# Kernel optimization log

Measured on AMD Instinct MI355X. Metric: run time of the kernel, lower is better.

## Reference

```python
import jax, jax.numpy as jnp
import numpy as np
from jax import lax

D_MODEL = 64      # feature_dim
D_STATE = 16      # state_dim
D_CONV = 4        # conv_dim
EXPAND = 2
D_INNER = EXPAND * D_MODEL          # 128
DT_RANK = (D_MODEL + 15) // 16      # ceil(d_model/16) = 4, mamba default
IN_DIM = 64
LN_EPS = 1e-3                        # keras LayerNormalization default epsilon


def setup_inputs() -> dict:
    key = jax.random.key(0)
    ks = jax.random.split(key, 12)
    B, L = 16, 8192
    s = 0.02
    x = jax.random.normal(ks[0], (B, L, IN_DIM), jnp.float32)
    W_in = jax.random.normal(ks[1], (IN_DIM, D_MODEL), jnp.float32) * s
    b_in = jnp.zeros((D_MODEL,), jnp.float32)
    in_proj_w = jax.random.normal(ks[2], (D_MODEL, 2 * D_INNER), jnp.float32) * s
    conv_w = jax.random.normal(ks[3], (D_INNER, D_CONV), jnp.float32) * 0.1
    conv_b = jnp.zeros((D_INNER,), jnp.float32)
    x_proj_w = jax.random.normal(ks[4], (D_INNER, DT_RANK + 2 * D_STATE), jnp.float32) * s
    dt_proj_w = jax.random.normal(ks[5], (DT_RANK, D_INNER), jnp.float32) * (DT_RANK ** -0.5)
    # dt bias init so softplus(dt) lands roughly in [dt_min, dt_max]
    dt = jnp.exp(jax.random.uniform(ks[6], (D_INNER,)) * (np.log(0.1) - np.log(0.001)) + np.log(0.001))
    dt_proj_b = dt + jnp.log(-jnp.expm1(-dt))  # inverse softplus
    A_log = jnp.log(jnp.broadcast_to(jnp.arange(1, D_STATE + 1, dtype=jnp.float32), (D_INNER, D_STATE)))
    D_skip = jnp.ones((D_INNER,), jnp.float32)
    out_proj_w = jax.random.normal(ks[7], (D_INNER, D_MODEL), jnp.float32) * s
    ln_gamma = jnp.ones((D_MODEL,), jnp.float32)
    ln_beta = jnp.zeros((D_MODEL,), jnp.float32)
    return {"x": x, "W_in": W_in, "b_in": b_in, "in_proj_w": in_proj_w,
            "conv_w": conv_w, "conv_b": conv_b, "x_proj_w": x_proj_w,
            "dt_proj_w": dt_proj_w, "dt_proj_b": dt_proj_b, "A_log": A_log,
            "D_skip": D_skip, "out_proj_w": out_proj_w,
            "ln_gamma": ln_gamma, "ln_beta": ln_beta}


def reference(x, W_in, b_in, in_proj_w, conv_w, conv_b, x_proj_w,
              dt_proj_w, dt_proj_b, A_log, D_skip, out_proj_w, ln_gamma, ln_beta):
    B, L, _ = x.shape
    # Conv1D kernel_size=1 input projection
    xin = x @ W_in + b_in                          # [B,L,D_MODEL]
    # --- Mamba ---
    xz = xin @ in_proj_w                           # [B,L,2*D_INNER]
    xc, z = xz[..., :D_INNER], xz[..., D_INNER:]
    # causal depthwise conv (groups=d_inner, padding=d_conv-1, crop to L)
    xp = jnp.pad(xc, ((0, 0), (D_CONV - 1, 0), (0, 0)))
    xconv = conv_b
    for k in range(D_CONV):
        xconv = xconv + xp[:, k:k + L, :] * conv_w[:, k]
    u = jax.nn.silu(xconv)                         # [B,L,D_INNER]
    dbc = u @ x_proj_w                             # [B,L,DT_RANK+2*D_STATE]
    dt = jax.nn.softplus(dbc[..., :DT_RANK] @ dt_proj_w + dt_proj_b)   # [B,L,D_INNER]
    Bm = dbc[..., DT_RANK:DT_RANK + D_STATE]       # [B,L,D_STATE]
    Cm = dbc[..., DT_RANK + D_STATE:]              # [B,L,D_STATE]
    A = -jnp.exp(A_log)                            # [D_INNER,D_STATE]

    def step(h, xs):
        dt_t, b_t, c_t, u_t = xs                   # [B,Di],[B,Ds],[B,Ds],[B,Di]
        dA = jnp.exp(dt_t[:, :, None] * A)         # [B,Di,Ds]
        h = dA * h + (dt_t * u_t)[:, :, None] * b_t[:, None, :]
        y = jnp.einsum('bds,bs->bd', h, c_t)
        return h, y

    xs = (jnp.swapaxes(dt, 0, 1), jnp.swapaxes(Bm, 0, 1),
          jnp.swapaxes(Cm, 0, 1), jnp.swapaxes(u, 0, 1))
    h0 = jnp.zeros((B, D_INNER, D_STATE), x.dtype)
    _, ys = lax.scan(step, h0, xs)                 # ys: [L,B,D_INNER]
    y = jnp.swapaxes(ys, 0, 1) + u * D_skip
    y = y * jax.nn.silu(z)
    h_out = y @ out_proj_w                         # [B,L,D_MODEL]
    # residual + LayerNorm
    res = h_out + xin
    mu = jnp.mean(res, axis=-1, keepdims=True)
    var = jnp.mean(jnp.square(res - mu), axis=-1, keepdims=True)
    return ln_gamma * (res - mu) * lax.rsqrt(var + LN_EPS) + ln_beta
```

## Files before the change

kernel.cpp:

```cpp
#include <hip/hip_runtime.h>
#include <hip/hip_bf16.h>

#define B_SZ   16
#define L_SZ   8192
#define DM     64
#define DI     128
#define NCH    128
#define CLEN   64
#define CH     64
#define RT     80
#define PA     72
#define PU     136
#define PC     132
#define LN_EPS 1e-3f

typedef float  f4 __attribute__((ext_vector_type(4)));
typedef short  s8 __attribute__((ext_vector_type(8)));
typedef unsigned short u16;
typedef unsigned int   u32;
#define MFMA16 __builtin_amdgcn_mfma_f32_16x16x32_bf16

__device__ __forceinline__ u16 f2bfu(float f) {
    u32 u = __float_as_uint(f);
    return (u16)((u + 0x7FFFu + ((u >> 16) & 1u)) >> 16);
}
__device__ __forceinline__ u32 pk2bf(float a, float b) {
    return (u32)f2bfu(a) | ((u32)f2bfu(b) << 16);
}
__device__ __forceinline__ float bflo(u32 u) { return __uint_as_float(u << 16); }
__device__ __forceinline__ float bfhi(u32 u) { return __uint_as_float(u & 0xFFFF0000u); }
__device__ __forceinline__ float bfu2f(u16 h) { return __uint_as_float((u32)h << 16); }
__device__ __forceinline__ float fsig(float v) {
    return __builtin_amdgcn_rcpf(1.f + __expf(-v));
}
__device__ __forceinline__ float fsp(float v) {
    return fmaxf(v, 0.f) + __logf(1.f + __expf(-fabsf(v)));
}

__global__ __launch_bounds__(256) void k_prep(
    const float* __restrict__ W_in, const float* __restrict__ in_proj,
    const float* __restrict__ x_proj, const float* __restrict__ Wout,
    u16* __restrict__ Wf1, u16* __restrict__ Wf2,
    u16* __restrict__ Wf3, u16* __restrict__ Wf4)
{
    const int tid = threadIdx.x;
    for (int g = tid; g < 512; g += 256) {
        int lane = g & 63, ks = (g >> 6) & 1, nt = g >> 7;
        int n = nt * 16 + (lane & 15), kb = ks * 32 + (lane >> 4) * 8;
        for (int j = 0; j < 8; j++) Wf1[g * 8 + j] = f2bfu(W_in[(kb + j) * 64 + n]);
    }
    for (int g = tid; g < 2048; g += 256) {
        int lane = g & 63, ks = (g >> 6) & 1, nt = g >> 7;
        int n = nt * 16 + (lane & 15), kb = ks * 32 + (lane >> 4) * 8;
        for (int j = 0; j < 8; j++) Wf2[g * 8 + j] = f2bfu(in_proj[(kb + j) * 256 + n]);
    }
    for (int g = tid; g < 768; g += 256) {
        int lane = g & 63, ks = (g >> 6) & 3, nt = g >> 8;
        int n = nt * 16 + (lane & 15), kb = ks * 32 + (lane >> 4) * 8;
        for (int j = 0; j < 8; j++)
            Wf3[g * 8 + j] = f2bfu(n < 36 ? x_proj[(kb + j) * 36 + n] : 0.f);
    }
    for (int g = tid; g < 1024; g += 256) {
        int lane = g & 63, ks = (g >> 6) & 3, nt = g >> 8;
        int n = nt * 16 + (lane & 15), kb = ks * 32 + (lane >> 4) * 8;
        for (int j = 0; j < 8; j++) Wf4[g * 8 + j] = f2bfu(Wout[(kb + j) * 64 + n]);
    }
}

__global__ __launch_bounds__(256) void k_frontend(
    const float* __restrict__ x, const float* __restrict__ b_in,
    const float* __restrict__ conv_w, const float* __restrict__ conv_b,
    const u16* __restrict__ Wf1, const u16* __restrict__ Wf2, const u16* __restrict__ Wf3,
    float* __restrict__ xin_g, u16* __restrict__ u_g, float* __restrict__ dtr_g,
    float* __restrict__ B_g, float* __restrict__ C_g, u16* __restrict__ sz_g)
{
    __shared__ __align__(16) char sm[41088];
    u16*   smA   = (u16*)sm;
    u16*   smB   = (u16*)(sm + 11520);
    u16*   smU   = (u16*)sm;
    float* smDtr = (float*)(sm + 17408);
    u16*   smC   = (u16*)(sm + 23040);

    const int tid = threadIdx.x;
    const int w = tid >> 6, lane = tid & 63;
    const int n16 = lane & 15, quad = lane >> 4;
    const int b = blockIdx.y, c0 = blockIdx.x * CH;
    const long long tokbase = (long long)b * L_SZ + c0;

    for (int idx = tid; idx < RT * 16; idx += 256) {
        int r = idx >> 4, c4 = idx & 15;
        int l = c0 - 3 + r;
        float4 v = make_float4(0.f, 0.f, 0.f, 0.f);
        if (r < 67 && l >= 0)
            v = *(const float4*)(x + ((long long)b * L_SZ + l) * 64 + c4 * 4);
        *(uint2*)((char*)smA + r * 144 + c4 * 8) = make_uint2(pk2bf(v.x, v.y), pk2bf(v.z, v.w));
    }
    __syncthreads();

    {
        s8 b0 = *(const s8*)(Wf1 + ((w * 2 + 0) * 64 + lane) * 8);
        s8 b1 = *(const s8*)(Wf1 + ((w * 2 + 1) * 64 + lane) * 8);
        float bias = b_in[w * 16 + n16];
        for (int m = 0; m < 5; m++) {
            int ar = m * 16 + n16;
            s8 a0 = *(const s8*)(smA + ar * PA + quad * 8);
            s8 a1 = *(const s8*)(smA + ar * PA + 32 + quad * 8);
            f4 acc = {0.f, 0.f, 0.f, 0.f};
            acc = MFMA16(a0, b0, acc, 0, 0, 0);
            acc = MFMA16(a1, b1, acc, 0, 0, 0);
#pragma unroll
            for (int reg = 0; reg < 4; reg++) {
                int rr = m * 16 + quad * 4 + reg;
                float v = acc[reg] + bias;
                smB[rr * PA + w * 16 + n16] = f2bfu(v);
                if (rr >= 3 && rr < 67)
                    xin_g[(tokbase + rr - 3) * 64 + w * 16 + n16] = v;
            }
        }
    }
    __syncthreads();

    {
        s8 bf[4][2];
#pragma unroll
        for (int i = 0; i < 4; i++)
#pragma unroll
            for (int ks = 0; ks < 2; ks++)
                bf[i][ks] = *(const s8*)(Wf2 + (((w * 4 + i) * 2 + ks) * 64 + lane) * 8);
        for (int m = 0; m < 5; m++) {
            int ar = m * 16 + n16;
            s8 a0 = *(const s8*)(smB + ar * PA + quad * 8);
            s8 a1 = *(const s8*)(smB + ar * PA + 32 + quad * 8);
#pragma unroll
            for (int i = 0; i < 4; i++) {
                f4 acc = {0.f, 0.f, 0.f, 0.f};
                acc = MFMA16(a0, bf[i][0], acc, 0, 0, 0);
                acc = MFMA16(a1, bf[i][1], acc, 0, 0, 0);
                int cg = (w * 4 + i) * 16 + n16;
#pragma unroll
                for (int reg = 0; reg < 4; reg++) {
                    int rr = m * 16 + quad * 4 + reg;
                    float v = acc[reg];
                    if (cg < 128) {
                        if (rr < 67) {
                            int l = c0 - 3 + rr;
                            smC[rr * PC + cg] = f2bfu(l >= 0 ? v : 0.f);
                        }
                    } else if (rr >= 3 && rr < 67) {
                        sz_g[(tokbase + rr - 3) * 128 + (cg - 128)] = f2bfu(v * fsig(v));
                    }
                }
            }
        }
    }
    __syncthreads();

    {
        const int d2 = lane * 2, ctb = w * 16;
        float4 cw0 = ((const float4*)conv_w)[d2];
        float4 cw1 = ((const float4*)conv_w)[d2 + 1];
        float cb0 = conv_b[d2], cb1 = conv_b[d2 + 1];
        u32 r0 = *(const u32*)((char*)smC + (ctb + 0) * 264 + lane * 4);
        u32 r1 = *(const u32*)((char*)smC + (ctb + 1) * 264 + lane * 4);
        u32 r2 = *(const u32*)((char*)smC + (ctb + 2) * 264 + lane * 4);
#pragma unroll 4
        for (int j = 0; j < 16; j++) {
            int ct = ctb + j;
            u32 r3 = *(const u32*)((char*)smC + (ct + 3) * 264 + lane * 4);
            float v0 = cb0 + bflo(r0) * cw0.x + bflo(r1) * cw0.y + bflo(r2) * cw0.z + bflo(r3) * cw0.w;
            float v1 = cb1 + bfhi(r0) * cw1.x + bfhi(r1) * cw1.y + bfhi(r2) * cw1.z + bfhi(r3) * cw1.w;
            u32 pk = pk2bf(v0 * fsig(v0), v1 * fsig(v1));
            *(u32*)(u_g + (tokbase + ct) * 128 + d2) = pk;
            *(u32*)(smU + ct * PU + d2) = pk;
            r0 = r1; r1 = r2; r2 = r3;
        }
    }
    __syncthreads();

    {
        s8 bf3[3][4];
#pragma unroll
        for (int nt = 0; nt < 3; nt++)
#pragma unroll
            for (int ks = 0; ks < 4; ks++)
                bf3[nt][ks] = *(const s8*)(Wf3 + ((nt * 4 + ks) * 64 + lane) * 8);
        f4 acc[3] = {{0.f,0.f,0.f,0.f},{0.f,0.f,0.f,0.f},{0.f,0.f,0.f,0.f}};
        int ar = w * 16 + n16;
#pragma unroll
        for (int ks = 0; ks < 4; ks++) {
            s8 a = *(const s8*)(smU + ar * PU + ks * 32 + quad * 8);
#pragma unroll
            for (int nt = 0; nt < 3; nt++) acc[nt] = MFMA16(a, bf3[nt][ks], acc[nt], 0, 0, 0);
        }
#pragma unroll
        for (int nt = 0; nt < 3; nt++) {
            int c = nt * 16 + n16;
#pragma unroll
            for (int reg = 0; reg < 4; reg++) {
                int rr = w * 16 + quad * 4 + reg;
                float v = acc[nt][reg];
                long long t = tokbase + rr;
                if (c < 4)       smDtr[rr * 4 + c] = v;
                else if (c < 20) B_g[t * 16 + (c - 4)] = v;
                else if (c < 36) C_g[t * 16 + (c - 20)] = v;
            }
        }
    }
    __syncthreads();

    if (tid < 64)
        *(float4*)(dtr_g + (tokbase + tid) * 4) = *(const float4*)(smDtr + tid * 4);
}

__global__ __launch_bounds__(128) void k_scan1(
    const float* __restrict__ dtr_g, const u16* __restrict__ u_g,
    const float* __restrict__ B_g, const float* __restrict__ A_log,
    const float* __restrict__ dt_w, const float* __restrict__ dt_b,
    float* __restrict__ hl_ws, float* __restrict__ sdt_ws)
{
    __shared__ __align__(16) float smQ[CLEN * 4];
    __shared__ __align__(16) float smBs[CLEN * 16];

    const int d = threadIdx.x, c = blockIdx.x, b = blockIdx.y;
    const long long tok0 = (long long)b * L_SZ + (long long)c * CLEN;

    {
        const float4* srcB = (const float4*)(B_g + tok0 * 16);
        float4* dstB = (float4*)smBs;
        dstB[d] = srcB[d];
        dstB[d + 128] = srcB[d + 128];
        if (d < 64) ((float4*)smQ)[d] = ((const float4*)(dtr_g + tok0 * 4))[d];
    }
    __syncthreads();

    const float w0 = dt_w[d], w1 = dt_w[128 + d], w2 = dt_w[256 + d], w3 = dt_w[384 + d];
    const float bdt = dt_b[d];

    float A[16];
#pragma unroll
    for (int s = 0; s < 16; s++) A[s] = -__expf(A_log[d * 16 + s]);
    const float A0 = A[0];
    bool chain = true;
#pragma unroll
    for (int s = 1; s < 16; s++)
        chain = chain && (fabsf(A[s] - (float)(s + 1) * A0) <= 1e-4f * fabsf(A[s]));

    float h[16];
#pragma unroll
    for (int s = 0; s < 16; s++) h[s] = 0.f;
    float sdt = 0.f;

    if (chain) {
        for (int i = 0; i < CLEN; i++) {
            float4 q = *(const float4*)(smQ + i * 4);
            float dtv = fsp(bdt + q.x * w0 + q.y * w1 + q.z * w2 + q.w * w3);
            float uv  = bfu2f(u_g[(tok0 + i) * 128 + d]);
            float4 b0 = *(const float4*)(smBs + i * 16);
            float4 b1 = *(const float4*)(smBs + i * 16 + 4);
            float4 b2 = *(const float4*)(smBs + i * 16 + 8);
            float4 b3 = *(const float4*)(smBs + i * 16 + 12);
            float Bv[16] = { b0.x, b0.y, b0.z, b0.w, b1.x, b1.y, b1.z, b1.w,
                             b2.x, b2.y, b2.z, b2.w, b3.x, b3.y, b3.z, b3.w };
            float du = dtv * uv;  sdt += dtv;
            float p = __expf(dtv * A0), dA = p;
            h[0] = dA * h[0] + du * Bv[0];
#pragma unroll
            for (int s = 1; s < 16; s++) { dA *= p; h[s] = dA * h[s] + du * Bv[s]; }
        }
    } else {
        for (int i = 0; i < CLEN; i++) {
            float4 q = *(const float4*)(smQ + i * 4);
            float dtv = fsp(bdt + q.x * w0 + q.y * w1 + q.z * w2 + q.w * w3);
            float uv  = bfu2f(u_g[(tok0 + i) * 128 + d]);
            float4 b0 = *(const float4*)(smBs + i * 16);
            float4 b1 = *(const float4*)(smBs + i * 16 + 4);
            float4 b2 = *(const float4*)(smBs + i * 16 + 8);
            float4 b3 = *(const float4*)(smBs + i * 16 + 12);
            float Bv[16] = { b0.x, b0.y, b0.z, b0.w, b1.x, b1.y, b1.z, b1.w,
                             b2.x, b2.y, b2.z, b2.w, b3.x, b3.y, b3.z, b3.w };
            float du = dtv * uv;  sdt += dtv;
#pragma unroll
            for (int s = 0; s < 16; s++) h[s] = __expf(dtv * A[s]) * h[s] + du * Bv[s];
        }
    }

    float4* hp4 = (float4*)(hl_ws + (((long long)b * NCH + c) * 128 + d) * 16);
    hp4[0] = make_float4(h[0], h[1], h[2], h[3]);
    hp4[1] = make_float4(h[4], h[5], h[6], h[7]);
    hp4[2] = make_float4(h[8], h[9], h[10], h[11]);
    hp4[3] = make_float4(h[12], h[13], h[14], h[15]);
    sdt_ws[((long long)b * NCH + c) * 128 + d] = sdt;
}

__global__ __launch_bounds__(256) void k_combine(
    const float* __restrict__ A_log, const float* __restrict__ hl_ws,
    const float* __restrict__ sdt_ws, float* __restrict__ hin_ws)
{
    const int tid = threadIdx.x, lane = tid & 63;
    const int seg = tid & 3;
    const int sIdx = blockIdx.x * 64 + (tid >> 2);
    const int b = sIdx >> 11, rem = sIdx & 2047, d = rem >> 4;
    const float A = -__expf(A_log[rem]);
    const int cBeg = seg * 32;
    const long long hlBase  = ((long long)b * NCH) * 2048 + rem;
    const long long sdtBase = ((long long)b * NCH) * 128 + d;

    float hloc = 0.f, ssum = 0.f;
#pragma unroll 4
    for (int c = cBeg; c < cBeg + 32; c++) {
        float sd = sdt_ws[sdtBase + (long long)c * 128];
        ssum += sd;
        hloc = __expf(A * sd) * hloc + hl_ws[hlBase + (long long)c * 2048];
    }

    float H = 0.f;
    const int gbase = lane & ~3;
#pragma unroll
    for (int k = 0; k < 3; k++) {
        float hs = __shfl(hloc, gbase + k, 64);
        float ss = __shfl(ssum, gbase + k, 64);
        if (k < seg) H = hs + H * __expf(A * ss);
    }

    float h = H;
#pragma unroll 4
    for (int c = cBeg; c < cBeg + 32; c++) {
        hin_ws[hlBase + (long long)c * 2048] = h;
        float sd = sdt_ws[sdtBase + (long long)c * 128];
        h = __expf(A * sd) * h + hl_ws[hlBase + (long long)c * 2048];
    }
}

__global__ __launch_bounds__(128) void k_scan3(
    const float* __restrict__ dtr_g, const u16* __restrict__ u_g,
    const float* __restrict__ B_g, const float* __restrict__ C_g,
    const u16* __restrict__ sz_g, const float* __restrict__ A_log,
    const float* __restrict__ dt_w, const float* __restrict__ dt_b,
    const float* __restrict__ D_skip, const float* __restrict__ hin_ws,
    u16* __restrict__ y_g)
{
    __shared__ __align__(16) float smQ[CLEN * 4];
    __shared__ __align__(16) float smBs[CLEN * 16];
    __shared__ __align__(16) float smCs[CLEN * 16];

    const int d = threadIdx.x, c = blockIdx.x, b = blockIdx.y;
    const long long tok0 = (long long)b * L_SZ + (long long)c * CLEN;

    {
        const float4* srcB = (const float4*)(B_g + tok0 * 16);
        const float4* srcC = (const float4*)(C_g + tok0 * 16);
        ((float4*)smBs)[d] = srcB[d];
        ((float4*)smBs)[d + 128] = srcB[d + 128];
        ((float4*)smCs)[d] = srcC[d];
        ((float4*)smCs)[d + 128] = srcC[d + 128];
        if (d < 64) ((float4*)smQ)[d] = ((const float4*)(dtr_g + tok0 * 4))[d];
    }
    __syncthreads();

    const float w0 = dt_w[d], w1 = dt_w[128 + d], w2 = dt_w[256 + d], w3 = dt_w[384 + d];
    const float bdt = dt_b[d];

    float A[16];
#pragma unroll
    for (int s = 0; s < 16; s++) A[s] = -__expf(A_log[d * 16 + s]);
    const float A0 = A[0];
    bool chain = true;
#pragma unroll
    for (int s = 1; s < 16; s++)
        chain = chain && (fabsf(A[s] - (float)(s + 1) * A0) <= 1e-4f * fabsf(A[s]));

    float h[16];
    {
        const float4* hp = (const float4*)(hin_ws + (((long long)b * NCH + c) * 128 + d) * 16);
        float4 h0 = hp[0], h1 = hp[1], h2 = hp[2], h3 = hp[3];
        h[0]=h0.x; h[1]=h0.y; h[2]=h0.z; h[3]=h0.w;
        h[4]=h1.x; h[5]=h1.y; h[6]=h1.z; h[7]=h1.w;
        h[8]=h2.x; h[9]=h2.y; h[10]=h2.z; h[11]=h2.w;
        h[12]=h3.x; h[13]=h3.y; h[14]=h3.z; h[15]=h3.w;
    }
    const float Dv = D_skip[d];

    if (chain) {
        for (int i = 0; i < CLEN; i++) {
            float4 q = *(const float4*)(smQ + i * 4);
            float dtv = fsp(bdt + q.x * w0 + q.y * w1 + q.z * w2 + q.w * w3);
            float uv  = bfu2f(u_g[(tok0 + i) * 128 + d]);
            float4 b0 = *(const float4*)(smBs + i * 16);
            float4 b1 = *(const float4*)(smBs + i * 16 + 4);
            float4 b2 = *(const float4*)(smBs + i * 16 + 8);
            float4 b3 = *(const float4*)(smBs + i * 16 + 12);
            float Bv[16] = { b0.x, b0.y, b0.z, b0.w, b1.x, b1.y, b1.z, b1.w,
                             b2.x, b2.y, b2.z, b2.w, b3.x, b3.y, b3.z, b3.w };
            float4 c0v = *(const float4*)(smCs + i * 16);
            float4 c1v = *(const float4*)(smCs + i * 16 + 4);
            float4 c2v = *(const float4*)(smCs + i * 16 + 8);
            float4 c3v = *(const float4*)(smCs + i * 16 + 12);
            float Cv[16] = { c0v.x, c0v.y, c0v.z, c0v.w, c1v.x, c1v.y, c1v.z, c1v.w,
                             c2v.x, c2v.y, c2v.z, c2v.w, c3v.x, c3v.y, c3v.z, c3v.w };
            float du = dtv * uv;
            float p = __expf(dtv * A0), dA = p;
            h[0] = dA * h[0] + du * Bv[0];
            float ysum = h[0] * Cv[0];
#pragma unroll
            for (int s = 1; s < 16; s++) {
                dA *= p;
                h[s] = dA * h[s] + du * Bv[s];
                ysum += h[s] * Cv[s];
            }
            float szv = bfu2f(sz_g[(tok0 + i) * 128 + d]);
            y_g[(tok0 + i) * 128 + d] = f2bfu((ysum + uv * Dv) * szv);
        }
    } else {
        for (int i = 0; i < CLEN; i++) {
            float4 q = *(const float4*)(smQ + i * 4);
            float dtv = fsp(bdt + q.x * w0 + q.y * w1 + q.z * w2 + q.w * w3);
            float uv  = bfu2f(u_g[(tok0 + i) * 128 + d]);
            float4 b0 = *(const float4*)(smBs + i * 16);
            float4 b1 = *(const float4*)(smBs + i * 16 + 4);
            float4 b2 = *(const float4*)(smBs + i * 16 + 8);
            float4 b3 = *(const float4*)(smBs + i * 16 + 12);
            float Bv[16] = { b0.x, b0.y, b0.z, b0.w, b1.x, b1.y, b1.z, b1.w,
                             b2.x, b2.y, b2.z, b2.w, b3.x, b3.y, b3.z, b3.w };
            float4 c0v = *(const float4*)(smCs + i * 16);
            float4 c1v = *(const float4*)(smCs + i * 16 + 4);
            float4 c2v = *(const float4*)(smCs + i * 16 + 8);
            float4 c3v = *(const float4*)(smCs + i * 16 + 12);
            float Cv[16] = { c0v.x, c0v.y, c0v.z, c0v.w, c1v.x, c1v.y, c1v.z, c1v.w,
                             c2v.x, c2v.y, c2v.z, c2v.w, c3v.x, c3v.y, c3v.z, c3v.w };
            float du = dtv * uv;
            float ysum = 0.f;
#pragma unroll
            for (int s = 0; s < 16; s++) {
                h[s] = __expf(dtv * A[s]) * h[s] + du * Bv[s];
                ysum += h[s] * Cv[s];
            }
            float szv = bfu2f(sz_g[(tok0 + i) * 128 + d]);
            y_g[(tok0 + i) * 128 + d] = f2bfu((ysum + uv * Dv) * szv);
        }
    }
}

__global__ __launch_bounds__(256) void k_epilogue(
    const u16* __restrict__ y_g, const float* __restrict__ xin_g,
    const u16* __restrict__ Wf4, const float* __restrict__ gamma,
    const float* __restrict__ beta, float* __restrict__ out)
{
    __shared__ __align__(16) char sm[34048];
    u16*   yA  = (u16*)sm;
    float* smR = (float*)(sm + 17408);

    const int tid = threadIdx.x;
    const int w = tid >> 6, lane = tid & 63;
    const int n16 = lane & 15, quad = lane >> 4;
    const long long t0 = (long long)blockIdx.x * 64;

    for (int idx = tid; idx < 64 * 64; idx += 256) {
        int r = idx >> 6, cp = idx & 63;
        u32 v = ((const u32*)y_g)[(t0 + r) * 64 + cp];
        *(u32*)((char*)yA + r * 272 + cp * 4) = v;
    }
    __syncthreads();

    {
        s8 bf[4];
#pragma unroll
        for (int ks = 0; ks < 4; ks++)
            bf[ks] = *(const s8*)(Wf4 + ((w * 4 + ks) * 64 + lane) * 8);
#pragma unroll
        for (int m = 0; m < 4; m++) {
            int ar = m * 16 + n16;
            f4 acc = {0.f, 0.f, 0.f, 0.f};
#pragma unroll
            for (int ks = 0; ks < 4; ks++) {
                s8 a = *(const s8*)(yA + ar * PU + ks * 32 + quad * 8);
                acc = MFMA16(a, bf[ks], acc, 0, 0, 0);
            }
#pragma unroll
            for (int reg = 0; reg < 4; reg++) {
                int rr = m * 16 + quad * 4 + reg;
                smR[rr * 65 + w * 16 + n16] = acc[reg];
            }
        }
    }
    __syncthreads();

    {
        int o = tid & 63, wv = tid >> 6;
        float g = gamma[o], bb = beta[o];
        for (int j = 0; j < 16; j++) {
            int rr = wv * 16 + j;
            float r = smR[rr * 65 + o] + xin_g[(t0 + rr) * 64 + o];
            float s = r;
#pragma unroll
            for (int mS = 0; mS < 6; mS++) s += __shfl_xor(s, 1 << mS, 64);
            float mu = s * (1.f / 64.f);
            float dv = r - mu;
            float vs = dv * dv;
#pragma unroll
            for (int mS = 0; mS < 6; mS++) vs += __shfl_xor(vs, 1 << mS, 64);
            out[(t0 + rr) * 64 + o] = g * dv * rsqrtf(vs * (1.f / 64.f) + LN_EPS) + bb;
        }
    }
}

extern "C" void kernel_launch(void* const* d_in, const int* in_sizes, int n_in,
                              void* d_out, int out_size, void* d_ws, size_t ws_size,
                              hipStream_t stream)
{
    const float* x       = (const float*)d_in[0];
    const float* W_in    = (const float*)d_in[1];
    const float* b_in    = (const float*)d_in[2];
    const float* in_proj = (const float*)d_in[3];
    const float* conv_w  = (const float*)d_in[4];
    const float* conv_b  = (const float*)d_in[5];
    const float* x_proj  = (const float*)d_in[6];
    const float* dt_w    = (const float*)d_in[7];
    const float* dt_b    = (const float*)d_in[8];
    const float* A_log   = (const float*)d_in[9];
    const float* D_skip  = (const float*)d_in[10];
    const float* Wout    = (const float*)d_in[11];
    const float* gamma   = (const float*)d_in[12];
    const float* beta    = (const float*)d_in[13];
    float* out = (float*)d_out;

    const long long NT = (long long)B_SZ * L_SZ;
    char* ws = (char*)d_ws;
    float*  xin_g = (float*)ws;   ws += NT * 64 * 4;
    float*  dtr_g = (float*)ws;   ws += NT * 4 * 4;
    float*  B_g   = (float*)ws;   ws += NT * 16 * 4;
    float*  C_g   = (float*)ws;   ws += NT * 16 * 4;
    u16*    u_g   = (u16*)ws;     ws += NT * 128 * 2;
    u16*    sz_g  = (u16*)ws;     ws += NT * 128 * 2;
    u16*    y_g   = (u16*)ws;     ws += NT * 128 * 2;
    float*  hl_ws  = (float*)ws;  ws += (long long)B_SZ * NCH * 2048 * 4;
    float*  sdt_ws = (float*)ws;  ws += (long long)B_SZ * NCH * 128 * 4;
    float*  hin_ws = (float*)ws;  ws += (long long)B_SZ * NCH * 2048 * 4;
    u16* Wf1 = (u16*)ws; ws += 4096 * 2;
    u16* Wf2 = (u16*)ws; ws += 16384 * 2;
    u16* Wf3 = (u16*)ws; ws += 6144 * 2;
    u16* Wf4 = (u16*)ws; ws += 8192 * 2;

    k_prep<<<1, 256, 0, stream>>>(W_in, in_proj, x_proj, Wout, Wf1, Wf2, Wf3, Wf4);

    k_frontend<<<dim3(L_SZ / CH, B_SZ), 256, 0, stream>>>(
        x, b_in, conv_w, conv_b, Wf1, Wf2, Wf3,
        xin_g, u_g, dtr_g, B_g, C_g, sz_g);

    k_scan1<<<dim3(NCH, B_SZ), 128, 0, stream>>>(
        dtr_g, u_g, B_g, A_log, dt_w, dt_b, hl_ws, sdt_ws);

    k_combine<<<512, 256, 0, stream>>>(A_log, hl_ws, sdt_ws, hin_ws);

    k_scan3<<<dim3(NCH, B_SZ), 128, 0, stream>>>(
        dtr_g, u_g, B_g, C_g, sz_g, A_log, dt_w, dt_b, D_skip, hin_ws, y_g);

    k_epilogue<<<2048, 256, 0, stream>>>(y_g, xin_g, Wf4, gamma, beta, out);
}
```

Measured before the change: 315.6 us.

## Fuse scan output pass with out-projection and LayerNorm epilogue

Merges the second scan pass and the epilogue kernel into one kernel. Each 64-token chunk's gated y stays in shared memory as bf16 and feeds the MFMA out-projection and LayerNorm directly, so the y_g global round trip and one launch go away. The serial dA*=p chain is replaced by a log-depth power tree, which shortens the dependency chain. The costs are a 128-thread block doing the whole epilogue with less parallelism, and heavier shared-memory and register use.

```diff
diff --git a/kernel.cpp b/kernel.cpp
--- a/kernel.cpp
+++ b/kernel.cpp
@@ -212,6 +212,14 @@
         *(float4*)(dtr_g + (tokbase + tid) * 4) = *(const float4*)(smDtr + tid * 4);
 }
 
+#define POWERS(p)                                                    \
+    float p2 = p * p, p3 = p2 * p, p4 = p2 * p2;                     \
+    float p8 = p4 * p4, p12 = p8 * p4;                               \
+    float dA0 = p,        dA1 = p2,       dA2 = p3,       dA3 = p4;  \
+    float dA4 = p4 * p,   dA5 = p4 * p2,  dA6 = p4 * p3,  dA7 = p8;  \
+    float dA8 = p8 * p,   dA9 = p8 * p2,  dA10 = p8 * p3, dA11 = p12;\
+    float dA12 = p12 * p, dA13 = p12 * p2, dA14 = p12 * p3, dA15 = p12 * p4;
+
 __global__ __launch_bounds__(128) void k_scan1(
     const float* __restrict__ dtr_g, const u16* __restrict__ u_g,
     const float* __restrict__ B_g, const float* __restrict__ A_log,
@@ -251,36 +259,48 @@
     float sdt = 0.f;
 
     if (chain) {
+        const u16* pu = u_g + tok0 * 128 + d;
+        const float* pq = smQ;
+        const float* pb = smBs;
+#pragma unroll 2
         for (int i = 0; i < CLEN; i++) {
-            float4 q = *(const float4*)(smQ + i * 4);
+            float4 q = *(const float4*)pq;  pq += 4;
             float dtv = fsp(bdt + q.x * w0 + q.y * w1 + q.z * w2 + q.w * w3);
-            float uv  = bfu2f(u_g[(tok0 + i) * 128 + d]);
-            float4 b0 = *(const float4*)(smBs + i * 16);
-            float4 b1 = *(const float4*)(smBs + i * 16 + 4);
-            float4 b2 = *(const float4*)(smBs + i * 16 + 8);
-            float4 b3 = *(const float4*)(smBs + i * 16 + 12);
-            float Bv[16] = { b0.x, b0.y, b0.z, b0.w, b1.x, b1.y, b1.z, b1.w,
-                             b2.x, b2.y, b2.z, b2.w, b3.x, b3.y, b3.z, b3.w };
+            float uv  = bfu2f(*pu);  pu += 128;
+            float4 b0 = ((const float4*)pb)[0];
+            float4 b1 = ((const float4*)pb)[1];
+            float4 b2 = ((const float4*)pb)[2];
+            float4 b3 = ((const float4*)pb)[3];
+            pb += 16;
             float du = dtv * uv;  sdt += dtv;
-            float p = __expf(dtv * A0), dA = p;
-            h[0] = dA * h[0] + du * Bv[0];
-#pragma unroll
-            for (int s = 1; s < 16; s++) { dA *= p; h[s] = dA * h[s] + du * Bv[s]; }
+            float p = __expf(dtv * A0);
+            POWERS(p)
+            h[0]  = dA0  * h[0]  + du * b0.x;
+            h[1]  = dA1  * h[1]  + du * b0.y;
+            h[2]  = dA2  * h[2]  + du * b0.z;
+            h[3]  = dA3  * h[3]  + du * b0.w;
+            h[4]  = dA4  * h[4]  + du * b1.x;
+            h[5]  = dA5  * h[5]  + du * b1.y;
+            h[6]  = dA6  * h[6]  + du * b1.z;
+            h[7]  = dA7  * h[7]  + du * b1.w;
+            h[8]  = dA8  * h[8]  + du * b2.x;
+            h[9]  = dA9  * h[9]  + du * b2.y;
+            h[10] = dA10 * h[10] + du * b2.z;
+            h[11] = dA11 * h[11] + du * b2.w;
+            h[12] = dA12 * h[12] + du * b3.x;
+            h[13] = dA13 * h[13] + du * b3.y;
+            h[14] = dA14 * h[14] + du * b3.z;
+            h[15] = dA15 * h[15] + du * b3.w;
         }
     } else {
         for (int i = 0; i < CLEN; i++) {
             float4 q = *(const float4*)(smQ + i * 4);
             float dtv = fsp(bdt + q.x * w0 + q.y * w1 + q.z * w2 + q.w * w3);
             float uv  = bfu2f(u_g[(tok0 + i) * 128 + d]);
-            float4 b0 = *(const float4*)(smBs + i * 16);
-            float4 b1 = *(const float4*)(smBs + i * 16 + 4);
-            float4 b2 = *(const float4*)(smBs + i * 16 + 8);
-            float4 b3 = *(const float4*)(smBs + i * 16 + 12);
-            float Bv[16] = { b0.x, b0.y, b0.z, b0.w, b1.x, b1.y, b1.z, b1.w,
-                             b2.x, b2.y, b2.z, b2.w, b3.x, b3.y, b3.z, b3.w };
             float du = dtv * uv;  sdt += dtv;
 #pragma unroll
-            for (int s = 0; s < 16; s++) h[s] = __expf(dtv * A[s]) * h[s] + du * Bv[s];
+            for (int s = 0; s < 16; s++)
+                h[s] = __expf(dtv * A[s]) * h[s] + du * smBs[i * 16 + s];
         }
     }
 
@@ -331,164 +351,174 @@
     }
 }
 
-__global__ __launch_bounds__(128) void k_scan3(
+__global__ __launch_bounds__(128) void k_scan3f(
     const float* __restrict__ dtr_g, const u16* __restrict__ u_g,
     const float* __restrict__ B_g, const float* __restrict__ C_g,
     const u16* __restrict__ sz_g, const float* __restrict__ A_log,
     const float* __restrict__ dt_w, const float* __restrict__ dt_b,
     const float* __restrict__ D_skip, const float* __restrict__ hin_ws,
-    u16* __restrict__ y_g)
+    const u16* __restrict__ Wf4, const float* __restrict__ xin_g,
+    const float* __restrict__ gamma, const float* __restrict__ beta,
+    float* __restrict__ out)
 {
-    __shared__ __align__(16) float smQ[CLEN * 4];
-    __shared__ __align__(16) float smBs[CLEN * 16];
-    __shared__ __align__(16) float smCs[CLEN * 16];
-
-    const int d = threadIdx.x, c = blockIdx.x, b = blockIdx.y;
-    const long long tok0 = (long long)b * L_SZ + (long long)c * CLEN;
-
-    {
-        const float4* srcB = (const float4*)(B_g + tok0 * 16);
-        const float4* srcC = (const float4*)(C_g + tok0 * 16);
+    __shared__ __align__(16) char sm[26624];
+    u16*   smY  = (u16*)sm;
+    float* smR  = (float*)sm;
+    float* smQ  = (float*)(sm + 17408);
+    float* smBs = (float*)(sm + 18432);
+    float* smCs = (float*)(sm + 22528);
+
+    const int tid = threadIdx.x;
+    const int d = tid, c = blockIdx.x, b = blockIdx.y;
+    const long long t0 = (long long)b * L_SZ + (long long)c * CLEN;
+
+    {
+        const float4* srcB = (const float4*)(B_g + t0 * 16);
+        const float4* srcC = (const float4*)(C_g + t0 * 16);
         ((float4*)smBs)[d] = srcB[d];
         ((float4*)smBs)[d + 128] = srcB[d + 128];
         ((float4*)smCs)[d] = srcC[d];
         ((float4*)smCs)[d + 128] = srcC[d + 128];
-        if (d < 64) ((float4*)smQ)[d] = ((const float4*)(dtr_g + tok0 * 4))[d];
-    }
-    __syncthreads();
-
-    const float w0 = dt_w[d], w1 = dt_w[128 + d], w2 = dt_w[256 + d], w3 = dt_w[384 + d];
-    const float bdt = dt_b[d];
-
-    float A[16];
-#pragma unroll
-    for (int s = 0; s < 16; s++) A[s] = -__expf(A_log[d * 16 + s]);
-    const float A0 = A[0];
-    bool chain = true;
-#pragma unroll
-    for (int s = 1; s < 16; s++)
-        chain = chain && (fabsf(A[s] - (float)(s + 1) * A0) <= 1e-4f * fabsf(A[s]));
-
-    float h[16];
-    {
-        const float4* hp = (const float4*)(hin_ws + (((long long)b * NCH + c) * 128 + d) * 16);
-        float4 h0 = hp[0], h1 = hp[1], h2 = hp[2], h3 = hp[3];
-        h[0]=h0.x; h[1]=h0.y; h[2]=h0.z; h[3]=h0.w;
-        h[4]=h1.x; h[5]=h1.y; h[6]=h1.z; h[7]=h1.w;
-        h[8]=h2.x; h[9]=h2.y; h[10]=h2.z; h[11]=h2.w;
-        h[12]=h3.x; h[13]=h3.y; h[14]=h3.z; h[15]=h3.w;
-    }
-    const float Dv = D_skip[d];
-
-    if (chain) {
-        for (int i = 0; i < CLEN; i++) {
-            float4 q = *(const float4*)(smQ + i * 4);
-            float dtv = fsp(bdt + q.x * w0 + q.y * w1 + q.z * w2 + q.w * w3);
-            float uv  = bfu2f(u_g[(tok0 + i) * 128 + d]);
-            float4 b0 = *(const float4*)(smBs + i * 16);
-            float4 b1 = *(const float4*)(smBs + i * 16 + 4);
-            float4 b2 = *(const float4*)(smBs + i * 16 + 8);
-            float4 b3 = *(const float4*)(smBs + i * 16 + 12);
-            float Bv[16] = { b0.x, b0.y, b0.z, b0.w, b1.x, b1.y, b1.z, b1.w,
-                             b2.x, b2.y, b2.z, b2.w, b3.x, b3.y, b3.z, b3.w };
-            float4 c0v = *(const float4*)(smCs + i * 16);
-            float4 c1v = *(const float4*)(smCs + i * 16 + 4);
-            float4 c2v = *(const float4*)(smCs + i * 16 + 8);
-            float4 c3v = *(const float4*)(smCs + i * 16 + 12);
-            float Cv[16] = { c0v.x, c0v.y, c0v.z, c0v.w, c1v.x, c1v.y, c1v.z, c1v.w,
-                             c2v.x, c2v.y, c2v.z, c2v.w, c3v.x, c3v.y, c3v.z, c3v.w };
-            float du = dtv * uv;
-            float p = __expf(dtv * A0), dA = p;
-            h[0] = dA * h[0] + du * Bv[0];
-            float ysum = h[0] * Cv[0];
-#pragma unroll
-            for (int s = 1; s < 16; s++) {
-                dA *= p;
-                h[s] = dA * h[s] + du * Bv[s];
-                ysum += h[s] * Cv[s];
-            }
-            float szv = bfu2f(sz_g[(tok0 + i) * 128 + d]);
-            y_g[(tok0 + i) * 128 + d] = f2bfu((ysum + uv * Dv) * szv);
-        }
-    } else {
-        for (int i = 0; i < CLEN; i++) {
-            float4 q = *(const float4*)(smQ + i * 4);
-            float dtv = fsp(bdt + q.x * w0 + q.y * w1 + q.z * w2 + q.w * w3);
-            float uv  = bfu2f(u_g[(tok0 + i) * 128 + d]);
-            float4 b0 = *(const float4*)(smBs + i * 16);
-            float4 b1 = *(const float4*)(smBs + i * 16 + 4);
-            float4 b2 = *(const float4*)(smBs + i * 16 + 8);
-            float4 b3 = *(const float4*)(smBs + i * 16 + 12);
-            float Bv[16] = { b0.x, b0.y, b0.z, b0.w, b1.x, b1.y, b1.z, b1.w,
-                             b2.x, b2.y, b2.z, b2.w, b3.x, b3.y, b3.z, b3.w };
-            float4 c0v = *(const float4*)(smCs + i * 16);
-            float4 c1v = *(const float4*)(smCs + i * 16 + 4);
-            float4 c2v = *(const float4*)(smCs + i * 16 + 8);
-            float4 c3v = *(const float4*)(smCs + i * 16 + 12);
-            float Cv[16] = { c0v.x, c0v.y, c0v.z, c0v.w, c1v.x, c1v.y, c1v.z, c1v.w,
-                             c2v.x, c2v.y, c2v.z, c2v.w, c3v.x, c3v.y, c3v.z, c3v.w };
-            float du = dtv * uv;
-            float ysum = 0.f;
-#pragma unroll
-            for (int s = 0; s < 16; s++) {
-                h[s] = __expf(dtv * A[s]) * h[s] + du * Bv[s];
-                ysum += h[s] * Cv[s];
-            }
-            float szv = bfu2f(sz_g[(tok0 + i) * 128 + d]);
-            y_g[(tok0 + i) * 128 + d] = f2bfu((ysum + uv * Dv) * szv);
-        }
-    }
-}
-
-__global__ __launch_bounds__(256) void k_epilogue(
-    const u16* __restrict__ y_g, const float* __restrict__ xin_g,
-    const u16* __restrict__ Wf4, const float* __restrict__ gamma,
-    const float* __restrict__ beta, float* __restrict__ out)
-{
-    __shared__ __align__(16) char sm[34048];
-    u16*   yA  = (u16*)sm;
-    float* smR = (float*)(sm + 17408);
-
-    const int tid = threadIdx.x;
+        if (d < 64) ((float4*)smQ)[d] = ((const float4*)(dtr_g + t0 * 4))[d];
+    }
+    __syncthreads();
+
+    {
+        const float w0 = dt_w[d], w1 = dt_w[128 + d], w2 = dt_w[256 + d], w3 = dt_w[384 + d];
+        const float bdt = dt_b[d];
+        float A[16];
+#pragma unroll
+        for (int s = 0; s < 16; s++) A[s] = -__expf(A_log[d * 16 + s]);
+        const float A0 = A[0];
+        bool chain = true;
+#pragma unroll
+        for (int s = 1; s < 16; s++)
+            chain = chain && (fabsf(A[s] - (float)(s + 1) * A0) <= 1e-4f * fabsf(A[s]));
+
+        float h[16];
+        {
+            const float4* hp = (const float4*)(hin_ws + (((long long)b * NCH + c) * 128 + d) * 16);
+            float4 h0 = hp[0], h1 = hp[1], h2 = hp[2], h3 = hp[3];
+            h[0]=h0.x; h[1]=h0.y; h[2]=h0.z; h[3]=h0.w;
+            h[4]=h1.x; h[5]=h1.y; h[6]=h1.z; h[7]=h1.w;
+            h[8]=h2.x; h[9]=h2.y; h[10]=h2.z; h[11]=h2.w;
+            h[12]=h3.x; h[13]=h3.y; h[14]=h3.z; h[15]=h3.w;
+        }
+        const float Dv = D_skip[d];
+
+        if (chain) {
+            const u16* pu = u_g + t0 * 128 + d;
+            const u16* psz = sz_g + t0 * 128 + d;
+            const float* pq = smQ;
+            const float* pb = smBs;
+            const float* pc = smCs;
+            u16* py = smY + d;
+            for (int i = 0; i < CLEN; i++) {
+                float4 q = *(const float4*)pq;  pq += 4;
+                float dtv = fsp(bdt + q.x * w0 + q.y * w1 + q.z * w2 + q.w * w3);
+                float uv  = bfu2f(*pu);  pu += 128;
+                float4 b0 = ((const float4*)pb)[0];
+                float4 b1 = ((const float4*)pb)[1];
+                float4 b2 = ((const float4*)pb)[2];
+                float4 b3 = ((const float4*)pb)[3];
+                pb += 16;
+                float4 c0 = ((const float4*)pc)[0];
+                float4 c1 = ((const float4*)pc)[1];
+                float4 c2 = ((const float4*)pc)[2];
+                float4 c3 = ((const float4*)pc)[3];
+                pc += 16;
+                float du = dtv * uv;
+                float p = __expf(dtv * A0);
+                POWERS(p)
+                h[0]  = dA0  * h[0]  + du * b0.x;
+                h[1]  = dA1  * h[1]  + du * b0.y;
+                h[2]  = dA2  * h[2]  + du * b0.z;
+                h[3]  = dA3  * h[3]  + du * b0.w;
+                h[4]  = dA4  * h[4]  + du * b1.x;
+                h[5]  = dA5  * h[5]  + du * b1.y;
+                h[6]  = dA6  * h[6]  + du * b1.z;
+                h[7]  = dA7  * h[7]  + du * b1.w;
+                h[8]  = dA8  * h[8]  + du * b2.x;
+                h[9]  = dA9  * h[9]  + du * b2.y;
+                h[10] = dA10 * h[10] + du * b2.z;
+                h[11] = dA11 * h[11] + du * b2.w;
+                h[12] = dA12 * h[12] + du * b3.x;
+                h[13] = dA13 * h[13] + du * b3.y;
+                h[14] = dA14 * h[14] + du * b3.z;
+                h[15] = dA15 * h[15] + du * b3.w;
+                float y0 = h[0]*c0.x + h[1]*c0.y + h[2]*c0.z + h[3]*c0.w;
+                float y1 = h[4]*c1.x + h[5]*c1.y + h[6]*c1.z + h[7]*c1.w;
+                float y2 = h[8]*c2.x + h[9]*c2.y + h[10]*c2.z + h[11]*c2.w;
+                float y3 = h[12]*c3.x + h[13]*c3.y + h[14]*c3.z + h[15]*c3.w;
+                float ysum = (y0 + y1) + (y2 + y3);
+                float szv = bfu2f(*psz);  psz += 128;
+                *py = f2bfu((ysum + uv * Dv) * szv);  py += PU;
+            }
+        } else {
+            for (int i = 0; i < CLEN; i++) {
+                float4 q = *(const float4*)(smQ + i * 4);
+                float dtv = fsp(bdt + q.x * w0 + q.y * w1 + q.z * w2 + q.w * w3);
+                float uv  = bfu2f(u_g[(t0 + i) * 128 + d]);
+                float du = dtv * uv;
+                float ysum = 0.f;
+#pragma unroll
+                for (int s = 0; s < 16; s++) {
+                    h[s] = __expf(dtv * A[s]) * h[s] + du * smBs[i * 16 + s];
+                    ysum += h[s] * smCs[i * 16 + s];
+                }
+                float szv = bfu2f(sz_g[(t0 + i) * 128 + d]);
+                smY[i * PU + d] = f2bfu((ysum + uv * Dv) * szv);
+            }
+        }
+    }
+    __syncthreads();
+
     const int w = tid >> 6, lane = tid & 63;
     const int n16 = lane & 15, quad = lane >> 4;
-    const long long t0 = (long long)blockIdx.x * 64;
-
-    for (int idx = tid; idx < 64 * 64; idx += 256) {
-        int r = idx >> 6, cp = idx & 63;
-        u32 v = ((const u32*)y_g)[(t0 + r) * 64 + cp];
-        *(u32*)((char*)yA + r * 272 + cp * 4) = v;
-    }
-    __syncthreads();
-
-    {
-        s8 bf[4];
-#pragma unroll
-        for (int ks = 0; ks < 4; ks++)
-            bf[ks] = *(const s8*)(Wf4 + ((w * 4 + ks) * 64 + lane) * 8);
+    f4 accs[4][2];
+    {
+        s8 bf[2][4];
+#pragma unroll
+        for (int j = 0; j < 2; j++)
+#pragma unroll
+            for (int ks = 0; ks < 4; ks++)
+                bf[j][ks] = *(const s8*)(Wf4 + (((2 * w + j) * 4 + ks) * 64 + lane) * 8);
 #pragma unroll
         for (int m = 0; m < 4; m++) {
             int ar = m * 16 + n16;
-            f4 acc = {0.f, 0.f, 0.f, 0.f};
-#pragma unroll
-            for (int ks = 0; ks < 4; ks++) {
-                s8 a = *(const s8*)(yA + ar * PU + ks * 32 + quad * 8);
-                acc = MFMA16(a, bf[ks], acc, 0, 0, 0);
-            }
+            s8 a[4];
+#pragma unroll
+            for (int ks = 0; ks < 4; ks++)
+                a[ks] = *(const s8*)(smY + ar * PU + ks * 32 + quad * 8);
+#pragma unroll
+            for (int j = 0; j < 2; j++) {
+                f4 acc = {0.f, 0.f, 0.f, 0.f};
+#pragma unroll
+                for (int ks = 0; ks < 4; ks++) acc = MFMA16(a[ks], bf[j][ks], acc, 0, 0, 0);
+                accs[m][j] = acc;
+            }
+        }
+    }
+    __syncthreads();
+
+#pragma unroll
+    for (int m = 0; m < 4; m++)
+#pragma unroll
+        for (int j = 0; j < 2; j++) {
+            int col = (2 * w + j) * 16 + n16;
 #pragma unroll
             for (int reg = 0; reg < 4; reg++) {
                 int rr = m * 16 + quad * 4 + reg;
-                smR[rr * 65 + w * 16 + n16] = acc[reg];
-            }
-        }
-    }
+                smR[rr * 65 + col] = accs[m][j][reg];
+            }
+        }
     __syncthreads();
 
     {
         int o = tid & 63, wv = tid >> 6;
         float g = gamma[o], bb = beta[o];
-        for (int j = 0; j < 16; j++) {
-            int rr = wv * 16 + j;
+        for (int j = 0; j < 32; j++) {
+            int rr = wv * 32 + j;
             float r = smR[rr * 65 + o] + xin_g[(t0 + rr) * 64 + o];
             float s = r;
 #pragma unroll
@@ -531,7 +561,6 @@
     float*  C_g   = (float*)ws;   ws += NT * 16 * 4;
     u16*    u_g   = (u16*)ws;     ws += NT * 128 * 2;
     u16*    sz_g  = (u16*)ws;     ws += NT * 128 * 2;
-    u16*    y_g   = (u16*)ws;     ws += NT * 128 * 2;
     float*  hl_ws  = (float*)ws;  ws += (long long)B_SZ * NCH * 2048 * 4;
     float*  sdt_ws = (float*)ws;  ws += (long long)B_SZ * NCH * 128 * 4;
     float*  hin_ws = (float*)ws;  ws += (long long)B_SZ * NCH * 2048 * 4;
@@ -551,8 +580,7 @@
 
     k_combine<<<512, 256, 0, stream>>>(A_log, hl_ws, sdt_ws, hin_ws);
 
-    k_scan3<<<dim3(NCH, B_SZ), 128, 0, stream>>>(
-        dtr_g, u_g, B_g, C_g, sz_g, A_log, dt_w, dt_b, D_skip, hin_ws, y_g);
-
-    k_epilogue<<<2048, 256, 0, stream>>>(y_g, xin_g, Wf4, gamma, beta, out);
-}
+    k_scan3f<<<dim3(NCH, B_SZ), 128, 0, stream>>>(
+        dtr_g, u_g, B_g, C_g, sz_g, A_log, dt_w, dt_b, D_skip, hin_ws,
+        Wf4, xin_g, gamma, beta, out);
+}
```

Result: slower. 330.1 us (+4.6%).
